# Optimization experiments

Hardware: AMD Instinct MI355X
Metric: run time of the kernel (lower is better)

Reference implementation:

```python
import jax, jax.numpy as jnp
import numpy as np

N_NODES = 100_000
N_EDGES = 3_200_000
IN_FEATS, N_HIDDEN, N_CLASSES = 512, 64, 32
ALPHA = 0.1
NITER = 10


def setup_inputs() -> dict:
    key = jax.random.key(0)
    kx, kw1, kw2, kr, kc = jax.random.split(key, 5)
    x = jax.random.normal(kx, (N_NODES, IN_FEATS), dtype=jnp.float32)
    w1 = jax.random.normal(kw1, (N_HIDDEN, IN_FEATS), dtype=jnp.float32) / np.sqrt(IN_FEATS)
    w2 = jax.random.normal(kw2, (N_CLASSES, N_HIDDEN), dtype=jnp.float32) / np.sqrt(N_HIDDEN)
    # random edges + self loops (A + I in calc_A_hat)
    r = jax.random.randint(kr, (N_EDGES,), 0, N_NODES, dtype=jnp.int32)
    c = jax.random.randint(kc, (N_EDGES,), 0, N_NODES, dtype=jnp.int32)
    loop = jnp.arange(N_NODES, dtype=jnp.int32)
    rows = jnp.concatenate([r, loop])
    cols = jnp.concatenate([c, loop])
    # symmetric-normalization values: (1-alpha) / sqrt(d[r]*d[c]); self loops guarantee d>=1
    deg = jax.ops.segment_sum(jnp.ones_like(rows, dtype=jnp.float32), rows, num_segments=N_NODES)
    vals = (1.0 - ALPHA) / jnp.sqrt(deg[rows] * deg[cols])
    return {"x": x, "w1": w1, "w2": w2, "rows": rows, "cols": cols, "vals": vals}


def reference(x, w1, w2, rows, cols, vals):
    n = x.shape[0]
    # 2-layer bias-free MLP (dropout is identity with drop_prob=None)
    h = jnp.tanh(x @ w1.T)                 # [N, H]
    local = h @ w2.T                       # [N, C]

    def spmm(p):
        # A_hat @ p via gather-multiply-scatter over the edge list
        return jax.ops.segment_sum(vals[:, None] * p[cols], rows, num_segments=n)

    def body(p, _):
        return spmm(p) + ALPHA * local, None

    preds, _ = jax.lax.scan(body, local, None, length=NITER)
    return preds
```

## Files before the change

### kernel.cpp

```cpp
#include <hip/hip_runtime.h>
#include <math.h>

#define IN_F 512
#define NH   64
#define NC   32
#define PPR_ALPHA 0.1f
#define NITER 10

#define CH        8192
#define RPB       64
#define RPB_SHIFT 6
#define BK_PAD    1792
#define SCAP      4096

typedef _Float16 half8 __attribute__((ext_vector_type(8)));
typedef _Float16 half4 __attribute__((ext_vector_type(4)));
typedef float f32x4 __attribute__((ext_vector_type(4)));

#define XP 40

__global__ __launch_bounds__(256) void k_mlp1(const float* __restrict__ x,
                                              const float* __restrict__ w1,
                                              float* __restrict__ h, int N) {
    __shared__ _Float16 xs[64 * XP] __attribute__((aligned(16)));
    __shared__ _Float16 wsd[64 * XP] __attribute__((aligned(16)));

    const int tid = threadIdx.x;
    const int wv  = tid >> 6;
    const int l   = tid & 63;
    const int n0  = blockIdx.x * 64;

    f32x4 acc[4];
#pragma unroll
    for (int ht = 0; ht < 4; ++ht) acc[ht] = (f32x4){0.f, 0.f, 0.f, 0.f};

    const int f4 = tid & 7;
    const int r0 = tid >> 3;

    const int m  = l & 15;
    const int kg = l >> 4;

    for (int kt = 0; kt < IN_F / 32; ++kt) {
        const int k0 = kt * 32;
        __syncthreads();
#pragma unroll
        for (int qq = 0; qq < 2; ++qq) {
            const int r = r0 + 32 * qq;
            int row = n0 + r; if (row >= N) row = N - 1;
            const float4 v = *(const float4*)(x + (size_t)row * IN_F + k0 + f4 * 4);
            half4 hv; hv[0] = (_Float16)v.x; hv[1] = (_Float16)v.y;
            hv[2] = (_Float16)v.z; hv[3] = (_Float16)v.w;
            *(half4*)&xs[r * XP + f4 * 4] = hv;
        }
#pragma unroll
        for (int qq = 0; qq < 2; ++qq) {
            const int hh = r0 + 32 * qq;
            const float4 v = *(const float4*)(w1 + (size_t)hh * IN_F + k0 + f4 * 4);
            half4 hv; hv[0] = (_Float16)v.x; hv[1] = (_Float16)v.y;
            hv[2] = (_Float16)v.z; hv[3] = (_Float16)v.w;
            *(half4*)&wsd[hh * XP + f4 * 4] = hv;
        }
        __syncthreads();

        const half8 a = *(const half8*)&xs[(wv * 16 + m) * XP + kg * 8];
#pragma unroll
        for (int ht = 0; ht < 4; ++ht) {
            const half8 b = *(const half8*)&wsd[(ht * 16 + m) * XP + kg * 8];
            acc[ht] = __builtin_amdgcn_mfma_f32_16x16x32_f16(a, b, acc[ht], 0, 0, 0);
        }
    }

    const int m4 = (l >> 4) * 4;
    const int hc = l & 15;
#pragma unroll
    for (int ht = 0; ht < 4; ++ht) {
#pragma unroll
        for (int rg = 0; rg < 4; ++rg) {
            const int row = n0 + wv * 16 + m4 + rg;
            if (row < N) h[(size_t)row * NH + ht * 16 + hc] = tanhf(acc[ht][rg]);
        }
    }
}

__global__ __launch_bounds__(256) void k_mlp2(const float* __restrict__ h,
                                              const float* __restrict__ w2,
                                              float* __restrict__ local, int N) {
    __shared__ float w2s[32 * 68];
    const int tid = threadIdx.x;
    {
        const int c = tid >> 3, f4 = tid & 7;
        *(float4*)&w2s[c * 68 + f4 * 4]       = *(const float4*)(w2 + c * NH + f4 * 4);
        *(float4*)&w2s[c * 68 + (f4 + 8) * 4] = *(const float4*)(w2 + c * NH + (f4 + 8) * 4);
    }
    __syncthreads();
    const int c = tid & 31, nl = tid >> 5;
    const int n = blockIdx.x * 8 + nl;
    if (n >= N) return;
    float acc = 0.f;
#pragma unroll
    for (int h4 = 0; h4 < NH / 4; ++h4) {
        const float4 hv = *(const float4*)(h + (size_t)n * NH + h4 * 4);
        const float4 wv = *(const float4*)&w2s[c * 68 + h4 * 4];
        acc += hv.x * wv.x + hv.y * wv.y + hv.z * wv.z + hv.w * wv.w;
    }
    local[(size_t)n * NC + c] = acc;
}

__global__ __launch_bounds__(256) void k_p1(const int* __restrict__ rows,
                                            const int* __restrict__ cols,
                                            const float* __restrict__ vals,
                                            float* __restrict__ s,
                                            int* __restrict__ M,
                                            int E, int nb, int nCh) {
    __shared__ int lh[BK_PAD];
    const int t = threadIdx.x;
    for (int i = t; i < BK_PAD; i += 256) lh[i] = 0;
    __syncthreads();
    const int base = blockIdx.x * CH;
    const int cE = min(CH, E - base);
    for (int i = t; i < cE; i += 256) {
        const int e = base + i;
        const int r = rows[e];
        atomicAdd(&lh[r >> RPB_SHIFT], 1);
        if (r == cols[e]) s[r] = sqrtf(vals[e] * (1.0f / (1.0f - PPR_ALPHA)));
    }
    __syncthreads();
    for (int b = t; b < nb; b += 256) M[(size_t)b * nCh + blockIdx.x] = lh[b];
}

__global__ __launch_bounds__(256) void k_bsum(const int* __restrict__ in,
                                              int* __restrict__ bsum, int L) {
    __shared__ int sdata[256];
    const int t = threadIdx.x;
    const int i = blockIdx.x * 256 + t;
    sdata[t] = (i < L) ? in[i] : 0;
    __syncthreads();
    for (int off = 128; off > 0; off >>= 1) {
        if (t < off) sdata[t] += sdata[t + off];
        __syncthreads();
    }
    if (t == 0) bsum[blockIdx.x] = sdata[0];
}

__global__ __launch_bounds__(1024) void k_scanb4(int* __restrict__ bsum, int NB) {
    __shared__ int sdata[1024];
    const int t = threadIdx.x;
    const int b0 = t * 4;
    int v[4], pre[4];
    int run = 0;
#pragma unroll
    for (int j = 0; j < 4; ++j) v[j] = (b0 + j < NB) ? bsum[b0 + j] : 0;
#pragma unroll
    for (int j = 0; j < 4; ++j) { pre[j] = run; run += v[j]; }
    sdata[t] = run;
    __syncthreads();
    for (int off = 1; off < 1024; off <<= 1) {
        const int add = (t >= off) ? sdata[t - off] : 0;
        __syncthreads();
        sdata[t] += add;
        __syncthreads();
    }
    const int base = sdata[t] - run;
#pragma unroll
    for (int j = 0; j < 4; ++j)
        if (b0 + j < NB) bsum[b0 + j] = base + pre[j];
}

__global__ __launch_bounds__(256) void k_scanf(const int* __restrict__ in,
                                               const int* __restrict__ bsum,
                                               int* __restrict__ S, int L) {
    __shared__ int sdata[256];
    const int t = threadIdx.x;
    const int i = blockIdx.x * 256 + t;
    const int v = (i < L) ? in[i] : 0;
    sdata[t] = v;
    __syncthreads();
    for (int off = 1; off < 256; off <<= 1) {
        const int add = (t >= off) ? sdata[t - off] : 0;
        __syncthreads();
        sdata[t] += add;
        __syncthreads();
    }
    if (i < L) S[i] = sdata[t] - v + bsum[blockIdx.x];
}

__global__ __launch_bounds__(256) void k_bin(const int* __restrict__ rows,
                                             const int* __restrict__ cols,
                                             const int* __restrict__ S,
                                             unsigned int* __restrict__ ep,
                                             int E, int nb, int nCh) {
    __shared__ unsigned int psorted[CH];
    __shared__ unsigned short sbuck[CH];
    __shared__ int bufA[BK_PAD];
    __shared__ int lstart[BK_PAD];
    __shared__ int tsum[256];

    const int t = threadIdx.x;
    const int chunk = blockIdx.x;
    const int base = chunk * CH;
    const int cE = min(CH, E - base);

    for (int i = t; i < BK_PAD; i += 256) bufA[i] = 0;
    __syncthreads();
    for (int i = t; i < cE; i += 256)
        atomicAdd(&bufA[rows[base + i] >> RPB_SHIFT], 1);
    __syncthreads();

    {
        const int b0 = t * 7;
        int pre[7];
        int run = 0;
#pragma unroll
        for (int j = 0; j < 7; ++j) { pre[j] = run; run += bufA[b0 + j]; }
        tsum[t] = run;
        __syncthreads();
        for (int off = 1; off < 256; off <<= 1) {
            const int add = (t >= off) ? tsum[t - off] : 0;
            __syncthreads();
            tsum[t] += add;
            __syncthreads();
        }
        const int ex = tsum[t] - run;
#pragma unroll
        for (int j = 0; j < 7; ++j) {
            const int vv = ex + pre[j];
            lstart[b0 + j] = vv;
            bufA[b0 + j] = vv;
        }
    }
    __syncthreads();

    for (int i = t; i < cE; i += 256) {
        const int e = base + i;
        const int r = rows[e];
        const int b = r >> RPB_SHIFT;
        const int pos = atomicAdd(&bufA[b], 1);
        psorted[pos] = ((unsigned)(r & (RPB - 1)) << 17) | (unsigned)cols[e];
        sbuck[pos] = (unsigned short)b;
    }
    __syncthreads();

    for (int b = t; b < nb; b += 256) bufA[b] = S[(size_t)b * nCh + chunk];
    __syncthreads();

    for (int i = t; i < cE; i += 256) {
        const int b = sbuck[i];
        ep[bufA[b] + (i - lstart[b])] = psorted[i];
    }
}

__global__ __launch_bounds__(256) void k_sort2(const unsigned int* __restrict__ ep,
                                               const int* __restrict__ S,
                                               unsigned int* __restrict__ ep2,
                                               int* __restrict__ rp,
                                               int E, int N, int nb, int nCh) {
    __shared__ unsigned int buf[SCAP];
    __shared__ unsigned int srt[SCAP];
    __shared__ int cnt[RPB];
    __shared__ int cur[RPB];

    const int t = threadIdx.x;
    const int b = blockIdx.x;
    const int estart = S[(size_t)b * nCh];
    const int eend = (b + 1 < nb) ? S[(size_t)(b + 1) * nCh] : E;
    const int ne = eend - estart;

    if (t < RPB) cnt[t] = 0;
    __syncthreads();
    for (int i = t; i < ne; i += 256) {
        const unsigned u = ep[estart + i];
        buf[i] = u;
        atomicAdd(&cnt[u >> 17], 1);
    }
    __syncthreads();
    if (t < RPB) {
        const int v = cnt[t];
        int x = v;
#pragma unroll
        for (int off = 1; off < RPB; off <<= 1) {
            const int y = __shfl_up(x, off);
            if (t >= off) x += y;
        }
        const int ex = x - v;
        cur[t] = ex;
        const int idx = b * RPB + t;
        if (idx <= N) rp[idx] = estart + ex;
    }
    __syncthreads();
    for (int i = t; i < ne; i += 256) {
        const unsigned u = buf[i];
        const int r = (int)(u >> 17);
        const int pos = atomicAdd(&cur[r], 1);
        srt[pos] = u & 0x1FFFFu;
    }
    __syncthreads();
    for (int i = t; i < ne; i += 256) ep2[estart + i] = srt[i];
}

__global__ __launch_bounds__(256) void k_q0(const float* __restrict__ local,
                                            const float* __restrict__ s,
                                            float* __restrict__ q, int N) {
    const int i = blockIdx.x * 256 + threadIdx.x;
    if (i < N * 8) {
        const int row = i >> 3;
        const float sr = s[row];
        float4 v = ((const float4*)local)[i];
        v.x *= sr; v.y *= sr; v.z *= sr; v.w *= sr;
        ((float4*)q)[i] = v;
    }
}

__global__ __launch_bounds__(256) void k_spmm(const int* __restrict__ rp,
                                              const unsigned int* __restrict__ ep2,
                                              const float* __restrict__ q,
                                              const float* __restrict__ localv,
                                              const float* __restrict__ s,
                                              float* __restrict__ dst,
                                              int N, int storeQ) {
    const int row = blockIdx.x * 8 + (threadIdx.x >> 5);
    if (row >= N) return;
    const int lane = threadIdx.x & 31;
    const int g  = lane >> 3;
    const int cq = lane & 7;
    const int e0 = rp[row], e1 = rp[row + 1];

    float4 accA = {0.f, 0.f, 0.f, 0.f};
    float4 accB = {0.f, 0.f, 0.f, 0.f};
    const int nIter = (e1 - e0 + 7) >> 3;
    for (int it = 0; it < nIter; ++it) {
        const int eA = e0 + it * 8 + g;
        const int eB = eA + 4;
        const unsigned cA = __builtin_nontemporal_load(&ep2[(eA < e1) ? eA : e0]);
        const unsigned cB = __builtin_nontemporal_load(&ep2[(eB < e1) ? eB : e0]);
        const float4 pA = *(const float4*)(q + (size_t)cA * NC + cq * 4);
        const float4 pB = *(const float4*)(q + (size_t)cB * NC + cq * 4);
        const float mA = (eA < e1) ? 1.f : 0.f;
        const float mB = (eB < e1) ? 1.f : 0.f;
        accA.x = fmaf(mA, pA.x, accA.x); accA.y = fmaf(mA, pA.y, accA.y);
        accA.z = fmaf(mA, pA.z, accA.z); accA.w = fmaf(mA, pA.w, accA.w);
        accB.x = fmaf(mB, pB.x, accB.x); accB.y = fmaf(mB, pB.y, accB.y);
        accB.z = fmaf(mB, pB.z, accB.z); accB.w = fmaf(mB, pB.w, accB.w);
    }
    float4 acc;
    acc.x = accA.x + accB.x; acc.y = accA.y + accB.y;
    acc.z = accA.z + accB.z; acc.w = accA.w + accB.w;
#pragma unroll
    for (int mask = 8; mask <= 16; mask <<= 1) {
        acc.x += __shfl_xor(acc.x, mask);
        acc.y += __shfl_xor(acc.y, mask);
        acc.z += __shfl_xor(acc.z, mask);
        acc.w += __shfl_xor(acc.w, mask);
    }
    if (g == 0) {
        const float sr = s[row];
        const float sc = (1.0f - PPR_ALPHA) * sr;
        const float4 lv = *(const float4*)(localv + (size_t)row * NC + cq * 4);
        float4 o;
        o.x = sc * acc.x + PPR_ALPHA * lv.x;
        o.y = sc * acc.y + PPR_ALPHA * lv.y;
        o.z = sc * acc.z + PPR_ALPHA * lv.z;
        o.w = sc * acc.w + PPR_ALPHA * lv.w;
        if (storeQ) { o.x *= sr; o.y *= sr; o.z *= sr; o.w *= sr; }
        *(float4*)(dst + (size_t)row * NC + cq * 4) = o;
    }
}

extern "C" void kernel_launch(void* const* d_in, const int* in_sizes, int n_in,
                              void* d_out, int out_size, void* d_ws, size_t ws_size,
                              hipStream_t stream) {
    const float* x    = (const float*)d_in[0];
    const float* w1   = (const float*)d_in[1];
    const float* w2   = (const float*)d_in[2];
    const int*   rows = (const int*)d_in[3];
    const int*   cols = (const int*)d_in[4];
    const float* vals = (const float*)d_in[5];

    const int N = in_sizes[0] / IN_F;
    const int E = in_sizes[3];
    const int nb  = (N + RPB - 1) >> RPB_SHIFT;
    const int nCh = (E + CH - 1) / CH;
    const int L   = nb * nCh;
    const int LB  = (L + 255) / 256;

    auto align16 = [](size_t v) { return (v + 15) & ~(size_t)15; };
    char* ws = (char*)d_ws;

    const size_t szH  = align16((size_t)N * NH * 4);
    const size_t szEp = align16((size_t)E * 4);
    const size_t szM  = align16((size_t)L * 4);
    const size_t szBs = align16((size_t)LB * 4);
    const size_t szQ  = align16((size_t)N * NC * 4);
    size_t szA = szH;
    if (szEp + szM + szBs > szA) szA = szEp + szM + szBs;
    if (2 * szQ > szA) szA = 2 * szQ;

    float*        hbuf = (float*)ws;
    unsigned int* ep   = (unsigned int*)ws;
    int*          M    = (int*)(ws + szEp);
    int*          bsum = (int*)(ws + szEp + szM);
    float*        qA   = (float*)ws;
    float*        qB   = (float*)(ws + szQ);
    size_t off = szA;
    unsigned int* ep2  = (unsigned int*)(ws + off); off += szEp;
    float* localb = (float*)(ws + off); off += align16((size_t)N * NC * 4);
    float* sbuf   = (float*)(ws + off); off += align16((size_t)N * 4);
    int*   rp     = (int*)(ws + off);   off += align16((size_t)(N + 1) * 4);
    (void)ws_size; (void)n_in; (void)out_size;

    k_mlp1<<<(N + 63) / 64, 256, 0, stream>>>(x, w1, hbuf, N);
    k_mlp2<<<(N + 7) / 8, 256, 0, stream>>>(hbuf, w2, localb, N);

    k_p1<<<nCh, 256, 0, stream>>>(rows, cols, vals, sbuf, M, E, nb, nCh);
    k_bsum<<<LB, 256, 0, stream>>>(M, bsum, L);
    k_scanb4<<<1, 1024, 0, stream>>>(bsum, LB);
    k_scanf<<<LB, 256, 0, stream>>>(M, bsum, M, L);
    k_bin<<<nCh, 256, 0, stream>>>(rows, cols, M, ep, E, nb, nCh);
    k_sort2<<<nb, 256, 0, stream>>>(ep, M, ep2, rp, E, N, nb, nCh);

    k_q0<<<(N * 8 + 255) / 256, 256, 0, stream>>>(localb, sbuf, qA, N);

    float* outp = (float*)d_out;
    const int spmm_grid = (N + 7) / 8;
    float* st[2] = {qA, qB};
    int cur = 0;
    for (int it = 1; it <= NITER; ++it) {
        const float* src = st[cur];
        float* dstp = (it < NITER) ? st[cur ^ 1] : outp;
        k_spmm<<<spmm_grid, 256, 0, stream>>>(rp, ep2, src, localb, sbuf, dstp,
                                              N, (it < NITER) ? 1 : 0);
        cur ^= 1;
    }
}
```

Baseline: 1.057 ms.

## Store propagated PPR vectors in fp16 and fuse q0 scaling into MLP2

The intermediate propagation vectors q are now stored in half precision, which halves the bytes gathered per edge in each SpMM iteration. Accumulation and the final output stay in fp32. The q0 scaling kernel is folded into k_mlp2, which now runs after k_p1 so the degree scale is available. The SpMM edge loop is unrolled to 4 gathers per lane per iteration to keep more loads in flight, at the cost of fp16 rounding error over 10 iterations.

```diff
diff --git a/kernel.cpp b/kernel.cpp
--- a/kernel.cpp
+++ b/kernel.cpp
@@ -84,7 +84,9 @@
 
 __global__ __launch_bounds__(256) void k_mlp2(const float* __restrict__ h,
                                               const float* __restrict__ w2,
-                                              float* __restrict__ local, int N) {
+                                              const float* __restrict__ s,
+                                              float* __restrict__ local,
+                                              _Float16* __restrict__ q0, int N) {
     __shared__ float w2s[32 * 68];
     const int tid = threadIdx.x;
     {
@@ -104,6 +106,7 @@
         acc += hv.x * wv.x + hv.y * wv.y + hv.z * wv.z + hv.w * wv.w;
     }
     local[(size_t)n * NC + c] = acc;
+    q0[(size_t)n * NC + c] = (_Float16)(acc * s[n]);
 }
 
 __global__ __launch_bounds__(256) void k_p1(const int* __restrict__ rows,
@@ -297,25 +300,13 @@
     for (int i = t; i < ne; i += 256) ep2[estart + i] = srt[i];
 }
 
-__global__ __launch_bounds__(256) void k_q0(const float* __restrict__ local,
-                                            const float* __restrict__ s,
-                                            float* __restrict__ q, int N) {
-    const int i = blockIdx.x * 256 + threadIdx.x;
-    if (i < N * 8) {
-        const int row = i >> 3;
-        const float sr = s[row];
-        float4 v = ((const float4*)local)[i];
-        v.x *= sr; v.y *= sr; v.z *= sr; v.w *= sr;
-        ((float4*)q)[i] = v;
-    }
-}
-
 __global__ __launch_bounds__(256) void k_spmm(const int* __restrict__ rp,
                                               const unsigned int* __restrict__ ep2,
-                                              const float* __restrict__ q,
+                                              const _Float16* __restrict__ q,
                                               const float* __restrict__ localv,
                                               const float* __restrict__ s,
-                                              float* __restrict__ dst,
+                                              _Float16* __restrict__ dstH,
+                                              float* __restrict__ dstF,
                                               int N, int storeQ) {
     const int row = blockIdx.x * 8 + (threadIdx.x >> 5);
     if (row >= N) return;
@@ -323,27 +314,42 @@
     const int g  = lane >> 3;
     const int cq = lane & 7;
     const int e0 = rp[row], e1 = rp[row + 1];
-
-    float4 accA = {0.f, 0.f, 0.f, 0.f};
-    float4 accB = {0.f, 0.f, 0.f, 0.f};
-    const int nIter = (e1 - e0 + 7) >> 3;
+    const int last = e1 - 1;
+
+    float4 a0 = {0.f, 0.f, 0.f, 0.f};
+    float4 a1 = {0.f, 0.f, 0.f, 0.f};
+    float4 a2 = {0.f, 0.f, 0.f, 0.f};
+    float4 a3 = {0.f, 0.f, 0.f, 0.f};
+    const int nIter = (e1 - e0 + 15) >> 4;
     for (int it = 0; it < nIter; ++it) {
-        const int eA = e0 + it * 8 + g;
-        const int eB = eA + 4;
-        const unsigned cA = __builtin_nontemporal_load(&ep2[(eA < e1) ? eA : e0]);
-        const unsigned cB = __builtin_nontemporal_load(&ep2[(eB < e1) ? eB : e0]);
-        const float4 pA = *(const float4*)(q + (size_t)cA * NC + cq * 4);
-        const float4 pB = *(const float4*)(q + (size_t)cB * NC + cq * 4);
+        const int eA = e0 + it * 16 + g;
+        const int eB = eA + 4, eC = eA + 8, eD = eA + 12;
+        const unsigned cA = __builtin_nontemporal_load(&ep2[(eA < e1) ? eA : last]);
+        const unsigned cB = __builtin_nontemporal_load(&ep2[(eB < e1) ? eB : last]);
+        const unsigned cC = __builtin_nontemporal_load(&ep2[(eC < e1) ? eC : last]);
+        const unsigned cD = __builtin_nontemporal_load(&ep2[(eD < e1) ? eD : last]);
+        const half4 vA = *(const half4*)(q + (size_t)cA * NC + cq * 4);
+        const half4 vB = *(const half4*)(q + (size_t)cB * NC + cq * 4);
+        const half4 vC = *(const half4*)(q + (size_t)cC * NC + cq * 4);
+        const half4 vD = *(const half4*)(q + (size_t)cD * NC + cq * 4);
         const float mA = (eA < e1) ? 1.f : 0.f;
         const float mB = (eB < e1) ? 1.f : 0.f;
-        accA.x = fmaf(mA, pA.x, accA.x); accA.y = fmaf(mA, pA.y, accA.y);
-        accA.z = fmaf(mA, pA.z, accA.z); accA.w = fmaf(mA, pA.w, accA.w);
-        accB.x = fmaf(mB, pB.x, accB.x); accB.y = fmaf(mB, pB.y, accB.y);
-        accB.z = fmaf(mB, pB.z, accB.z); accB.w = fmaf(mB, pB.w, accB.w);
+        const float mC = (eC < e1) ? 1.f : 0.f;
+        const float mD = (eD < e1) ? 1.f : 0.f;
+        a0.x = fmaf(mA, (float)vA[0], a0.x); a0.y = fmaf(mA, (float)vA[1], a0.y);
+        a0.z = fmaf(mA, (float)vA[2], a0.z); a0.w = fmaf(mA, (float)vA[3], a0.w);
+        a1.x = fmaf(mB, (float)vB[0], a1.x); a1.y = fmaf(mB, (float)vB[1], a1.y);
+        a1.z = fmaf(mB, (float)vB[2], a1.z); a1.w = fmaf(mB, (float)vB[3], a1.w);
+        a2.x = fmaf(mC, (float)vC[0], a2.x); a2.y = fmaf(mC, (float)vC[1], a2.y);
+        a2.z = fmaf(mC, (float)vC[2], a2.z); a2.w = fmaf(mC, (float)vC[3], a2.w);
+        a3.x = fmaf(mD, (float)vD[0], a3.x); a3.y = fmaf(mD, (float)vD[1], a3.y);
+        a3.z = fmaf(mD, (float)vD[2], a3.z); a3.w = fmaf(mD, (float)vD[3], a3.w);
     }
     float4 acc;
-    acc.x = accA.x + accB.x; acc.y = accA.y + accB.y;
-    acc.z = accA.z + accB.z; acc.w = accA.w + accB.w;
+    acc.x = (a0.x + a1.x) + (a2.x + a3.x);
+    acc.y = (a0.y + a1.y) + (a2.y + a3.y);
+    acc.z = (a0.z + a1.z) + (a2.z + a3.z);
+    acc.w = (a0.w + a1.w) + (a2.w + a3.w);
 #pragma unroll
     for (int mask = 8; mask <= 16; mask <<= 1) {
         acc.x += __shfl_xor(acc.x, mask);
@@ -360,8 +366,14 @@
         o.y = sc * acc.y + PPR_ALPHA * lv.y;
         o.z = sc * acc.z + PPR_ALPHA * lv.z;
         o.w = sc * acc.w + PPR_ALPHA * lv.w;
-        if (storeQ) { o.x *= sr; o.y *= sr; o.z *= sr; o.w *= sr; }
-        *(float4*)(dst + (size_t)row * NC + cq * 4) = o;
+        if (storeQ) {
+            half4 oh;
+            oh[0] = (_Float16)(o.x * sr); oh[1] = (_Float16)(o.y * sr);
+            oh[2] = (_Float16)(o.z * sr); oh[3] = (_Float16)(o.w * sr);
+            *(half4*)(dstH + (size_t)row * NC + cq * 4) = oh;
+        } else {
+            *(float4*)(dstF + (size_t)row * NC + cq * 4) = o;
+        }
     }
 }
 
@@ -389,45 +401,45 @@
     const size_t szEp = align16((size_t)E * 4);
     const size_t szM  = align16((size_t)L * 4);
     const size_t szBs = align16((size_t)LB * 4);
-    const size_t szQ  = align16((size_t)N * NC * 4);
-    size_t szA = szH;
-    if (szEp + szM + szBs > szA) szA = szEp + szM + szBs;
-    if (2 * szQ > szA) szA = 2 * szQ;
+    const size_t szQh = align16((size_t)N * NC * 2);
+    const size_t szA  = (szH > szEp) ? szH : szEp;
 
     float*        hbuf = (float*)ws;
     unsigned int* ep   = (unsigned int*)ws;
-    int*          M    = (int*)(ws + szEp);
-    int*          bsum = (int*)(ws + szEp + szM);
-    float*        qA   = (float*)ws;
-    float*        qB   = (float*)(ws + szQ);
     size_t off = szA;
+    int*          M    = (int*)(ws + off);          off += szM;
+    int*          bsum = (int*)(ws + off);          off += szBs;
     unsigned int* ep2  = (unsigned int*)(ws + off); off += szEp;
-    float* localb = (float*)(ws + off); off += align16((size_t)N * NC * 4);
-    float* sbuf   = (float*)(ws + off); off += align16((size_t)N * 4);
-    int*   rp     = (int*)(ws + off);   off += align16((size_t)(N + 1) * 4);
+    float*        localb = (float*)(ws + off);      off += align16((size_t)N * NC * 4);
+    _Float16*     qA   = (_Float16*)(ws + off);     off += szQh;
+    _Float16*     qB   = (_Float16*)(ws + off);     off += szQh;
+    float*        sbuf = (float*)(ws + off);        off += align16((size_t)N * 4);
+    int*          rp   = (int*)(ws + off);          off += align16((size_t)(N + 1) * 4);
     (void)ws_size; (void)n_in; (void)out_size;
 
     k_mlp1<<<(N + 63) / 64, 256, 0, stream>>>(x, w1, hbuf, N);
-    k_mlp2<<<(N + 7) / 8, 256, 0, stream>>>(hbuf, w2, localb, N);
-
     k_p1<<<nCh, 256, 0, stream>>>(rows, cols, vals, sbuf, M, E, nb, nCh);
+    k_mlp2<<<(N + 7) / 8, 256, 0, stream>>>(hbuf, w2, sbuf, localb, qA, N);
+
     k_bsum<<<LB, 256, 0, stream>>>(M, bsum, L);
     k_scanb4<<<1, 1024, 0, stream>>>(bsum, LB);
     k_scanf<<<LB, 256, 0, stream>>>(M, bsum, M, L);
     k_bin<<<nCh, 256, 0, stream>>>(rows, cols, M, ep, E, nb, nCh);
     k_sort2<<<nb, 256, 0, stream>>>(ep, M, ep2, rp, E, N, nb, nCh);
 
-    k_q0<<<(N * 8 + 255) / 256, 256, 0, stream>>>(localb, sbuf, qA, N);
-
     float* outp = (float*)d_out;
     const int spmm_grid = (N + 7) / 8;
-    float* st[2] = {qA, qB};
+    _Float16* st[2] = {qA, qB};
     int cur = 0;
     for (int it = 1; it <= NITER; ++it) {
-        const float* src = st[cur];
-        float* dstp = (it < NITER) ? st[cur ^ 1] : outp;
-        k_spmm<<<spmm_grid, 256, 0, stream>>>(rp, ep2, src, localb, sbuf, dstp,
-                                              N, (it < NITER) ? 1 : 0);
+        const _Float16* src = st[cur];
+        if (it < NITER) {
+            k_spmm<<<spmm_grid, 256, 0, stream>>>(rp, ep2, src, localb, sbuf,
+                                                  st[cur ^ 1], nullptr, N, 1);
+        } else {
+            k_spmm<<<spmm_grid, 256, 0, stream>>>(rp, ep2, src, localb, sbuf,
+                                                  nullptr, outp, N, 0);
+        }
         cur ^= 1;
     }
 }
```

After: 973.1 us. -8.0%, faster.
